# Kernel tuning notes

Measured on AMD Instinct MI355X. Metric: run time of the kernel, lower is better.

Reference implementation:

```python
import jax, jax.numpy as jnp
import numpy as np

N_LAYERS = 3
NUM_USERS = 100000
NUM_ITEMS = 50000
N_NODES = NUM_USERS + NUM_ITEMS
N_EDGES = 6000000
EMB = 64


def setup_inputs() -> dict:
    key = jax.random.key(0)
    k1, k2, k3, k4, k5, k6, k7 = jax.random.split(key, 7)
    user_indices = jax.random.randint(k1, (1024,), 0, NUM_USERS)
    item_indices = jax.random.randint(k2, (1024,), 0, NUM_ITEMS)
    adj_src = jax.random.randint(k3, (N_EDGES,), 0, N_NODES)
    adj_dst = jax.random.randint(k4, (N_EDGES,), 0, N_NODES)
    # normalized adjacency values (stand-in for D^-1/2 A D^-1/2 entries)
    adj_vals = jax.random.uniform(k5, (N_EDGES,), dtype=jnp.float32) * 0.05
    user_emb = jax.random.normal(k6, (NUM_USERS, EMB), dtype=jnp.float32) * 0.1
    item_emb = jax.random.normal(k7, (NUM_ITEMS, EMB), dtype=jnp.float32) * 0.1
    return {
        "user_indices": user_indices,
        "item_indices": item_indices,
        "adj_src": adj_src,
        "adj_dst": adj_dst,
        "adj_vals": adj_vals,
        "user_emb": user_emb,
        "item_emb": item_emb,
    }


def reference(user_indices, item_indices, adj_src, adj_dst, adj_vals, user_emb, item_emb):
    # LightGCN.computer(): all_emb = cat(users, items); repeated SpMM; mean over layers
    all_emb = jnp.concatenate([user_emb, item_emb], axis=0)  # [N, d]
    n = all_emb.shape[0]
    cur = all_emb
    acc = all_emb  # running sum over layer embeddings (fused, avoids stacking)
    for _ in range(N_LAYERS):
        # SpMM in COO form: out[dst] += val * cur[src]
        msgs = adj_vals[:, None] * cur[adj_src]  # [E, d]
        cur = jax.ops.segment_sum(msgs, adj_dst, num_segments=n)
        acc = acc + cur
    light_out = acc / jnp.float32(N_LAYERS + 1)  # mean over (n_layers+1) embeddings
    # forward() returns cat(all_users, all_items) == light_out
    return light_out
```

## Files before the change

### kernel.cpp

```cpp
#include <hip/hip_runtime.h>


#define NUM_USERS 100000
#define NUM_ITEMS 50000
#define N_NODES   150000
#define EMB       64
#define N_EDGES   6000000

#define ROWS_PER_B 256
#define NBUCKETS   586
#define NROWS_PAD  (NBUCKETS * ROWS_PER_B)
#define PART_BLOCKS 512
#define CHUNK ((N_EDGES + PART_BLOCKS - 1) / PART_BLOCKS)
#define CAP_B 10952

constexpr int NODE_F4 = N_NODES * EMB / 4;
constexpr int USER_F4 = NUM_USERS * EMB / 4;

typedef float f4v __attribute__((ext_vector_type(4)));

__device__ __forceinline__ float bf2f(unsigned short u) {
    union { unsigned int i; float f; } x; x.i = ((unsigned int)u) << 16; return x.f;
}
__device__ __forceinline__ unsigned short f2bf(float f) {
    union { float f; unsigned int i; } x; x.f = f;
    unsigned int b = x.i;
    return (unsigned short)((b + 0x7FFFu + ((b >> 16) & 1u)) >> 16);
}


__global__ void k_ginit(int* __restrict__ gcur) {
    int i = blockIdx.x * blockDim.x + threadIdx.x;
    if (i < NBUCKETS) gcur[i] = i * CAP_B;
}

__global__ __launch_bounds__(256) void k_part(const int* __restrict__ src,
                                              const int* __restrict__ dst,
                                              const float* __restrict__ val,
                                              int* __restrict__ gcur,
                                              int2* __restrict__ pairs) {
    __shared__ int cnt[NBUCKETS];
    __shared__ int base[NBUCKETS];
    int t = threadIdx.x;
    for (int i = t; i < NBUCKETS; i += 256) cnt[i] = 0;
    __syncthreads();
    int e0 = blockIdx.x * CHUNK;
    int e1 = min(e0 + CHUNK, N_EDGES);
    {
        int e = e0 + t;
        for (; e + 7 * 256 < e1; e += 8 * 256) {
            int b_[8];
#pragma unroll
            for (int j = 0; j < 8; ++j)
                b_[j] = __builtin_nontemporal_load(dst + e + j * 256) >> 8;
#pragma unroll
            for (int j = 0; j < 8; ++j) atomicAdd(&cnt[b_[j]], 1);
        }
        for (; e < e1; e += 256)
            atomicAdd(&cnt[__builtin_nontemporal_load(dst + e) >> 8], 1);
    }
    __syncthreads();
    for (int i = t; i < NBUCKETS; i += 256) {
        int c = cnt[i];
        base[i] = c ? atomicAdd(&gcur[i], c) : 0;
        cnt[i] = 0;
    }
    __syncthreads();
    {
        int e = e0 + t;
        for (; e + 7 * 256 < e1; e += 8 * 256) {
            int d_[8], s_[8];
            float v_[8];
#pragma unroll
            for (int j = 0; j < 8; ++j)
                d_[j] = __builtin_nontemporal_load(dst + e + j * 256);
#pragma unroll
            for (int j = 0; j < 8; ++j)
                s_[j] = __builtin_nontemporal_load(src + e + j * 256);
#pragma unroll
            for (int j = 0; j < 8; ++j)
                v_[j] = __builtin_nontemporal_load(val + e + j * 256);
#pragma unroll
            for (int j = 0; j < 8; ++j) {
                int b_ = d_[j] >> 8;
                int o = atomicAdd(&cnt[b_], 1);
                pairs[base[b_] + o] = make_int2(s_[j] | ((d_[j] & 255) << 18),
                                                __float_as_int(v_[j]));
            }
        }
        for (; e < e1; e += 256) {
            int d0 = __builtin_nontemporal_load(dst + e);
            int s0 = __builtin_nontemporal_load(src + e);
            float v0 = __builtin_nontemporal_load(val + e);
            int b_ = d0 >> 8;
            int o0 = atomicAdd(&cnt[b_], 1);
            pairs[base[b_] + o0] = make_int2(s0 | ((d0 & 255) << 18),
                                             __float_as_int(v0));
        }
    }
}

__global__ void k_fill(const int* __restrict__ gcur, int* __restrict__ boff) {
    __shared__ int s[1024];
    int t = threadIdx.x;
    int x = (t < NBUCKETS) ? (gcur[t] - t * CAP_B) : 0;
    s[t] = x;
    __syncthreads();
    for (int off = 1; off < 1024; off <<= 1) {
        int v = (t >= off) ? s[t - off] : 0;
        __syncthreads();
        s[t] += v;
        __syncthreads();
    }
    if (t < NBUCKETS) boff[t] = s[t] - x;
    if (t == 0) boff[NBUCKETS] = N_EDGES;
}

__global__ __launch_bounds__(1024) void k_sortA(const int* __restrict__ gcur,
                                                const int* __restrict__ boff,
                                                const int2* __restrict__ pairs1,
                                                int2* __restrict__ pairs2,
                                                int* __restrict__ row_ptr) {
    __shared__ int cnt[ROWS_PER_B];
    __shared__ int s[ROWS_PER_B];
    int b = blockIdx.x;
    int t = threadIdx.x;
    if (t < ROWS_PER_B) cnt[t] = 0;
    __syncthreads();
    int beg = b * CAP_B;
    int end = gcur[b];
    {
        int e = beg + t;
        for (; e + 7 * 1024 < end; e += 8 * 1024) {
            int r_[8];
#pragma unroll
            for (int j = 0; j < 8; ++j)
                r_[j] = ((unsigned)pairs1[e + j * 1024].x) >> 18;
#pragma unroll
            for (int j = 0; j < 8; ++j) atomicAdd(&cnt[r_[j]], 1);
        }
        for (; e < end; e += 1024)
            atomicAdd(&cnt[((unsigned)pairs1[e].x) >> 18], 1);
    }
    __syncthreads();
    int x = (t < ROWS_PER_B) ? cnt[t] : 0;
    if (t < ROWS_PER_B) s[t] = x;
    __syncthreads();
    for (int off = 1; off < ROWS_PER_B; off <<= 1) {
        int v = (t >= off && t < ROWS_PER_B) ? s[t - off] : 0;
        __syncthreads();
        if (t < ROWS_PER_B) s[t] += v;
        __syncthreads();
    }
    if (t < ROWS_PER_B) {
        int ex = boff[b] + s[t] - x;
        row_ptr[b * ROWS_PER_B + t] = ex;
        cnt[t] = ex;
    }
    if (b == NBUCKETS - 1 && t == 0) row_ptr[NROWS_PAD] = N_EDGES;
    __syncthreads();
    const long* p1l = (const long*)pairs1;
    {
        int e = beg + t;
        for (; e + 7 * 1024 < end; e += 8 * 1024) {
            long q[8];
#pragma unroll
            for (int j = 0; j < 8; ++j)
                q[j] = __builtin_nontemporal_load(p1l + e + j * 1024);
#pragma unroll
            for (int j = 0; j < 8; ++j) {
                int x0 = (int)q[j], y0 = (int)(q[j] >> 32);
                int pos = atomicAdd(&cnt[((unsigned)x0) >> 18], 1);
                pairs2[pos] = make_int2(x0 & 0x3FFFF, y0);
            }
        }
        for (; e < end; e += 1024) {
            long q0 = __builtin_nontemporal_load(p1l + e);
            int x0 = (int)q0, y0 = (int)(q0 >> 32);
            int pos = atomicAdd(&cnt[((unsigned)x0) >> 18], 1);
            pairs2[pos] = make_int2(x0 & 0x3FFFF, y0);
        }
    }
}


__global__ void k_zero(int* __restrict__ p, int n) {
    int i = blockIdx.x * blockDim.x + threadIdx.x;
    if (i < n) p[i] = 0;
}

__global__ __launch_bounds__(256) void k_bhist(const int* __restrict__ dst,
                                               int* __restrict__ gcnt,
                                               int* __restrict__ cnt_pb) {
    __shared__ int cnt[NBUCKETS];
    int t = threadIdx.x;
    for (int i = t; i < NBUCKETS; i += 256) cnt[i] = 0;
    __syncthreads();
    int e0 = blockIdx.x * CHUNK;
    int e1 = min(e0 + CHUNK, N_EDGES);
    int e = e0 + t;
    for (; e + 7 * 256 < e1; e += 8 * 256) {
        int b_[8];
#pragma unroll
        for (int j = 0; j < 8; ++j)
            b_[j] = __builtin_nontemporal_load(dst + e + j * 256) >> 8;
#pragma unroll
        for (int j = 0; j < 8; ++j) atomicAdd(&cnt[b_[j]], 1);
    }
    for (; e < e1; e += 256)
        atomicAdd(&cnt[__builtin_nontemporal_load(dst + e) >> 8], 1);
    __syncthreads();
    for (int i = t; i < NBUCKETS; i += 256) {
        int c = cnt[i];
        cnt_pb[blockIdx.x * NBUCKETS + i] = c;
        if (c) atomicAdd(&gcnt[i], c);
    }
}

__global__ void k_bscan(const int* __restrict__ gcnt, int* __restrict__ boff) {
    __shared__ int s[1024];
    int t = threadIdx.x;
    int x = (t < NBUCKETS) ? gcnt[t] : 0;
    s[t] = x;
    __syncthreads();
    for (int off = 1; off < 1024; off <<= 1) {
        int v = (t >= off) ? s[t - off] : 0;
        __syncthreads();
        s[t] += v;
        __syncthreads();
    }
    if (t < NBUCKETS) boff[t] = s[t] - x;
    if (t == 0) boff[NBUCKETS] = N_EDGES;
}

__global__ __launch_bounds__(512) void k_pscan(const int* __restrict__ boff,
                                               int* __restrict__ cnt_pb) {
    __shared__ int s[PART_BLOCKS];
    int k = blockIdx.x;
    int t = threadIdx.x;
    int x = cnt_pb[t * NBUCKETS + k];
    s[t] = x;
    __syncthreads();
    for (int off = 1; off < PART_BLOCKS; off <<= 1) {
        int v = (t >= off) ? s[t - off] : 0;
        __syncthreads();
        s[t] += v;
        __syncthreads();
    }
    cnt_pb[t * NBUCKETS + k] = boff[k] + s[t] - x;
}

__global__ __launch_bounds__(256) void k_part2(const int* __restrict__ src,
                                               const int* __restrict__ dst,
                                               const float* __restrict__ val,
                                               const int* __restrict__ cnt_pb,
                                               int2* __restrict__ pairs) {
    __shared__ int cnt[NBUCKETS];
    __shared__ int base[NBUCKETS];
    int t = threadIdx.x;
    for (int i = t; i < NBUCKETS; i += 256) {
        base[i] = cnt_pb[blockIdx.x * NBUCKETS + i];
        cnt[i] = 0;
    }
    __syncthreads();
    int e0 = blockIdx.x * CHUNK;
    int e1 = min(e0 + CHUNK, N_EDGES);
    int e = e0 + t;
    for (; e + 7 * 256 < e1; e += 8 * 256) {
        int d_[8], s_[8];
        float v_[8];
#pragma unroll
        for (int j = 0; j < 8; ++j)
            d_[j] = __builtin_nontemporal_load(dst + e + j * 256);
#pragma unroll
        for (int j = 0; j < 8; ++j)
            s_[j] = __builtin_nontemporal_load(src + e + j * 256);
#pragma unroll
        for (int j = 0; j < 8; ++j)
            v_[j] = __builtin_nontemporal_load(val + e + j * 256);
#pragma unroll
        for (int j = 0; j < 8; ++j) {
            int b_ = d_[j] >> 8;
            int o = atomicAdd(&cnt[b_], 1);
            pairs[base[b_] + o] = make_int2(s_[j] | ((d_[j] & 255) << 18),
                                            __float_as_int(v_[j]));
        }
    }
    for (; e < e1; e += 256) {
        int d0 = __builtin_nontemporal_load(dst + e);
        int s0 = __builtin_nontemporal_load(src + e);
        float v0 = __builtin_nontemporal_load(val + e);
        int b_ = d0 >> 8;
        int o0 = atomicAdd(&cnt[b_], 1);
        pairs[base[b_] + o0] = make_int2(s0 | ((d0 & 255) << 18),
                                         __float_as_int(v0));
    }
}

__global__ __launch_bounds__(512) void k_sort(const int* __restrict__ boff,
                                              const int2* __restrict__ pairs1,
                                              int2* __restrict__ pairs2,
                                              int* __restrict__ row_ptr) {
    __shared__ int cnt[ROWS_PER_B];
    __shared__ int s[ROWS_PER_B];
    int b = blockIdx.x;
    int t = threadIdx.x;
    if (t < ROWS_PER_B) cnt[t] = 0;
    __syncthreads();
    int beg = boff[b], end = boff[b + 1];
    {
        int e = beg + t;
        for (; e + 7 * 512 < end; e += 8 * 512) {
            int r_[8];
#pragma unroll
            for (int j = 0; j < 8; ++j)
                r_[j] = ((unsigned)pairs1[e + j * 512].x) >> 18;
#pragma unroll
            for (int j = 0; j < 8; ++j) atomicAdd(&cnt[r_[j]], 1);
        }
        for (; e < end; e += 512)
            atomicAdd(&cnt[((unsigned)pairs1[e].x) >> 18], 1);
    }
    __syncthreads();
    int x = (t < ROWS_PER_B) ? cnt[t] : 0;
    if (t < ROWS_PER_B) s[t] = x;
    __syncthreads();
    for (int off = 1; off < ROWS_PER_B; off <<= 1) {
        int v = (t >= off && t < ROWS_PER_B) ? s[t - off] : 0;
        __syncthreads();
        if (t < ROWS_PER_B) s[t] += v;
        __syncthreads();
    }
    if (t < ROWS_PER_B) {
        int ex = beg + s[t] - x;
        row_ptr[b * ROWS_PER_B + t] = ex;
        cnt[t] = ex;
    }
    if (b == NBUCKETS - 1 && t == 0) row_ptr[NROWS_PAD] = N_EDGES;
    __syncthreads();
    const long* p1l = (const long*)pairs1;
    {
        int e = beg + t;
        for (; e + 7 * 512 < end; e += 8 * 512) {
            long q[8];
#pragma unroll
            for (int j = 0; j < 8; ++j)
                q[j] = __builtin_nontemporal_load(p1l + e + j * 512);
#pragma unroll
            for (int j = 0; j < 8; ++j) {
                int x0 = (int)q[j], y0 = (int)(q[j] >> 32);
                int pos = atomicAdd(&cnt[((unsigned)x0) >> 18], 1);
                pairs2[pos] = make_int2(x0 & 0x3FFFF, y0);
            }
        }
        for (; e < end; e += 512) {
            long q0 = __builtin_nontemporal_load(p1l + e);
            int x0 = (int)q0, y0 = (int)(q0 >> 32);
            int pos = atomicAdd(&cnt[((unsigned)x0) >> 18], 1);
            pairs2[pos] = make_int2(x0 & 0x3FFFF, y0);
        }
    }
}


__global__ void k_init(const f4v* __restrict__ ue, const f4v* __restrict__ ie,
                       ushort4* __restrict__ e0b, f4v* __restrict__ acc) {
    int i = blockIdx.x * blockDim.x + threadIdx.x;
    if (i >= NODE_F4) return;
    f4v v = (i < USER_F4) ? __builtin_nontemporal_load(ue + i)
                          : __builtin_nontemporal_load(ie + i - USER_F4);
    __builtin_nontemporal_store(v, acc + i);
    e0b[i] = make_ushort4(f2bf(v.x), f2bf(v.y), f2bf(v.z), f2bf(v.w));
}

__global__ __launch_bounds__(256) void k_spmm(const int* __restrict__ row_ptr,
                                              const long* __restrict__ pairs,
                                              const ushort4* __restrict__ cur,
                                              ushort4* __restrict__ nxt) {
    int tid = blockIdx.x * blockDim.x + threadIdx.x;
    int row = tid >> 4;
    if (row >= N_NODES) return;
    int c = tid & 15;
    int beg = row_ptr[row];
    int end = row_ptr[row + 1];
    float4 r = make_float4(0.f, 0.f, 0.f, 0.f);
    int k = beg;
    for (; k + 7 < end; k += 8) {
        long p[8];
        ushort4 g[8];
#pragma unroll
        for (int j = 0; j < 8; ++j) p[j] = pairs[k + j];
#pragma unroll
        for (int j = 0; j < 8; ++j) g[j] = cur[(long)(int)(p[j] & 0x3FFFF) * 16 + c];
#pragma unroll
        for (int j = 0; j < 8; ++j) {
            float v = __int_as_float((int)(p[j] >> 32));
            r.x += v * bf2f(g[j].x);
            r.y += v * bf2f(g[j].y);
            r.z += v * bf2f(g[j].z);
            r.w += v * bf2f(g[j].w);
        }
    }
    for (; k < end; ++k) {
        long p0 = pairs[k];
        ushort4 g0 = cur[(long)(int)(p0 & 0x3FFFF) * 16 + c];
        float v0 = __int_as_float((int)(p0 >> 32));
        r.x += v0 * bf2f(g0.x);
        r.y += v0 * bf2f(g0.y);
        r.z += v0 * bf2f(g0.z);
        r.w += v0 * bf2f(g0.w);
    }
    nxt[(long)row * 16 + c] = make_ushort4(f2bf(r.x), f2bf(r.y), f2bf(r.z), f2bf(r.w));
}

__global__ __launch_bounds__(256) void k_spmm_fin(const int* __restrict__ row_ptr,
                                                  const long* __restrict__ pairs,
                                                  const ushort4* __restrict__ cur,
                                                  const ushort4* __restrict__ e1b,
                                                  float4* __restrict__ acc) {
    int tid = blockIdx.x * blockDim.x + threadIdx.x;
    int row = tid >> 4;
    if (row >= N_NODES) return;
    int c = tid & 15;
    int beg = row_ptr[row];
    int end = row_ptr[row + 1];
    float4 r = make_float4(0.f, 0.f, 0.f, 0.f);
    int k = beg;
    for (; k + 7 < end; k += 8) {
        long p[8];
        ushort4 g[8];
#pragma unroll
        for (int j = 0; j < 8; ++j) p[j] = pairs[k + j];
#pragma unroll
        for (int j = 0; j < 8; ++j) g[j] = cur[(long)(int)(p[j] & 0x3FFFF) * 16 + c];
#pragma unroll
        for (int j = 0; j < 8; ++j) {
            float v = __int_as_float((int)(p[j] >> 32));
            r.x += v * bf2f(g[j].x);
            r.y += v * bf2f(g[j].y);
            r.z += v * bf2f(g[j].z);
            r.w += v * bf2f(g[j].w);
        }
    }
    for (; k < end; ++k) {
        long p0 = pairs[k];
        ushort4 g0 = cur[(long)(int)(p0 & 0x3FFFF) * 16 + c];
        float v0 = __int_as_float((int)(p0 >> 32));
        r.x += v0 * bf2f(g0.x);
        r.y += v0 * bf2f(g0.y);
        r.z += v0 * bf2f(g0.z);
        r.w += v0 * bf2f(g0.w);
    }
    long o = (long)row * 16 + c;
    ushort4 e1 = e1b[o];
    ushort4 e2 = cur[o];
    float4 a = acc[o];
    a.x = (a.x + bf2f(e1.x) + bf2f(e2.x) + r.x) * 0.25f;
    a.y = (a.y + bf2f(e1.y) + bf2f(e2.y) + r.y) * 0.25f;
    a.z = (a.z + bf2f(e1.z) + bf2f(e2.z) + r.z) * 0.25f;
    a.w = (a.w + bf2f(e1.w) + bf2f(e2.w) + r.w) * 0.25f;
    acc[o] = a;
}


__global__ void lgcn_init(const float4* __restrict__ user_emb,
                          const float4* __restrict__ item_emb,
                          float4* __restrict__ cur, float4* __restrict__ nxt,
                          float4* __restrict__ acc) {
    int i = blockIdx.x * blockDim.x + threadIdx.x;
    if (i >= NODE_F4) return;
    float4 v = (i < USER_F4) ? user_emb[i] : item_emb[i - USER_F4];
    cur[i] = v; acc[i] = v; nxt[i] = make_float4(0.f, 0.f, 0.f, 0.f);
}

__global__ void lgcn_scatter(const int* __restrict__ src, const int* __restrict__ dst,
                             const float* __restrict__ val,
                             const float4* __restrict__ cur, float* __restrict__ nxt) {
    int tid = blockIdx.x * blockDim.x + threadIdx.x;
    int e = tid >> 4;
    if (e >= N_EDGES) return;
    int c = tid & 15;
    int s = src[e]; int d = dst[e]; float v = val[e];
    float4 m = cur[(long)s * 16 + c];
    float* p = nxt + (long)d * 64 + c * 4;
    unsafeAtomicAdd(p + 0, v * m.x);
    unsafeAtomicAdd(p + 1, v * m.y);
    unsafeAtomicAdd(p + 2, v * m.z);
    unsafeAtomicAdd(p + 3, v * m.w);
}

__global__ void lgcn_add_zero(float4* __restrict__ acc, const float4* __restrict__ nxt,
                              float4* __restrict__ other) {
    int i = blockIdx.x * blockDim.x + threadIdx.x;
    if (i >= NODE_F4) return;
    float4 a = acc[i]; float4 n = nxt[i];
    a.x += n.x; a.y += n.y; a.z += n.z; a.w += n.w;
    acc[i] = a;
    other[i] = make_float4(0.f, 0.f, 0.f, 0.f);
}

__global__ void lgcn_final(float4* __restrict__ acc, const float4* __restrict__ nxt) {
    int i = blockIdx.x * blockDim.x + threadIdx.x;
    if (i >= NODE_F4) return;
    float4 a = acc[i]; float4 n = nxt[i];
    a.x = (a.x + n.x) * 0.25f; a.y = (a.y + n.y) * 0.25f;
    a.z = (a.z + n.z) * 0.25f; a.w = (a.w + n.w) * 0.25f;
    acc[i] = a;
}


extern "C" void kernel_launch(void* const* d_in, const int* in_sizes, int n_in,
                              void* d_out, int out_size, void* d_ws, size_t ws_size,
                              hipStream_t stream) {
    const int*    adj_src  = (const int*)d_in[2];
    const int*    adj_dst  = (const int*)d_in[3];
    const float*  adj_vals = (const float*)d_in[4];
    float* acc = (float*)d_out;

    const int BLK = 256;
    const int grid_node  = (NODE_F4 + BLK - 1) / BLK;
    const int grid_row16 = (N_NODES * 16 + BLK - 1) / BLK;

    const size_t SZ_PAIRS = (size_t)N_EDGES * 8;
    const size_t SZ_P1PAD = (size_t)NBUCKETS * CAP_B * 8;
    const size_t SZ_BF    = (size_t)N_NODES * EMB * 2;
    const size_t SZ_RP    = 600320;
    const size_t SZ_B     = 4096;
    const size_t NEEDED1  = SZ_PAIRS + SZ_P1PAD + SZ_BF + SZ_RP + 2 * SZ_B;
    const size_t NEEDED2  = 2 * SZ_PAIRS + SZ_BF + SZ_RP + 3 * SZ_B;

    if (ws_size >= NEEDED1) {
        char* w = (char*)d_ws;
        int2*    pairs2 = (int2*)(w);
        int2*    pairs1 = (int2*)(w + SZ_PAIRS);
        ushort4* e0b    = (ushort4*)(w + SZ_PAIRS);
        ushort4* e1b    = (ushort4*)(w + SZ_PAIRS + SZ_BF);
        ushort4* e2b    = (ushort4*)(w + SZ_PAIRS + SZ_P1PAD);
        int*  row_ptr= (int*)(w + SZ_PAIRS + SZ_P1PAD + SZ_BF);
        int*  gcur   = (int*)(w + SZ_PAIRS + SZ_P1PAD + SZ_BF + SZ_RP);
        int*  boff   = (int*)(w + SZ_PAIRS + SZ_P1PAD + SZ_BF + SZ_RP + SZ_B);

        k_ginit<<<(NBUCKETS + BLK - 1) / BLK, BLK, 0, stream>>>(gcur);
        k_part<<<PART_BLOCKS, BLK, 0, stream>>>(adj_src, adj_dst, adj_vals,
                                                gcur, pairs1);
        k_fill<<<1, 1024, 0, stream>>>(gcur, boff);
        k_sortA<<<NBUCKETS, 1024, 0, stream>>>(gcur, boff, pairs1, pairs2, row_ptr);

        k_init<<<grid_node, BLK, 0, stream>>>((const f4v*)d_in[5], (const f4v*)d_in[6],
                                              e0b, (f4v*)acc);
        k_spmm<<<grid_row16, BLK, 0, stream>>>(row_ptr, (const long*)pairs2, e0b, e1b);
        k_spmm<<<grid_row16, BLK, 0, stream>>>(row_ptr, (const long*)pairs2, e1b, e2b);
        k_spmm_fin<<<grid_row16, BLK, 0, stream>>>(row_ptr, (const long*)pairs2, e2b,
                                                   e1b, (float4*)acc);
    } else if (ws_size >= NEEDED2) {
        char* w = (char*)d_ws;
        int2*    pairs2 = (int2*)(w);
        int*     cnt_pb = (int*)(w);
        int2*    pairs1 = (int2*)(w + SZ_PAIRS);
        ushort4* e0b    = (ushort4*)(w + SZ_PAIRS);
        ushort4* e1b    = (ushort4*)(w + SZ_PAIRS + SZ_BF);
        ushort4* e2b    = (ushort4*)(w + 2 * SZ_PAIRS);
        int*  row_ptr= (int*)(w + 2 * SZ_PAIRS + SZ_BF);
        int*  gcnt   = (int*)(w + 2 * SZ_PAIRS + SZ_BF + SZ_RP);
        int*  boff   = (int*)(w + 2 * SZ_PAIRS + SZ_BF + SZ_RP + SZ_B);

        k_zero<<<(NBUCKETS + BLK - 1) / BLK, BLK, 0, stream>>>(gcnt, NBUCKETS);
        k_bhist<<<PART_BLOCKS, BLK, 0, stream>>>(adj_dst, gcnt, cnt_pb);
        k_bscan<<<1, 1024, 0, stream>>>(gcnt, boff);
        k_pscan<<<NBUCKETS, PART_BLOCKS, 0, stream>>>(boff, cnt_pb);
        k_part2<<<PART_BLOCKS, BLK, 0, stream>>>(adj_src, adj_dst, adj_vals,
                                                 cnt_pb, pairs1);
        k_sort<<<NBUCKETS, 512, 0, stream>>>(boff, pairs1, pairs2, row_ptr);

        k_init<<<grid_node, BLK, 0, stream>>>((const f4v*)d_in[5], (const f4v*)d_in[6],
                                              e0b, (f4v*)acc);
        k_spmm<<<grid_row16, BLK, 0, stream>>>(row_ptr, (const long*)pairs2, e0b, e1b);
        k_spmm<<<grid_row16, BLK, 0, stream>>>(row_ptr, (const long*)pairs2, e1b, e2b);
        k_spmm_fin<<<grid_row16, BLK, 0, stream>>>(row_ptr, (const long*)pairs2, e2b,
                                                   e1b, (float4*)acc);
    } else {
        const float4* user_emb = (const float4*)d_in[5];
        const float4* item_emb = (const float4*)d_in[6];
        float* ws0 = (float*)d_ws;
        float* ws1 = ws0 + (size_t)N_NODES * EMB;
        lgcn_init<<<grid_node, BLK, 0, stream>>>(user_emb, item_emb,
                                                 (float4*)ws0, (float4*)ws1, (float4*)acc);
        lgcn_scatter<<<(N_EDGES*16+BLK-1)/BLK, BLK, 0, stream>>>(adj_src, adj_dst, adj_vals,
                                                    (const float4*)ws0, ws1);
        lgcn_add_zero<<<grid_node, BLK, 0, stream>>>((float4*)acc, (const float4*)ws1, (float4*)ws0);
        lgcn_scatter<<<(N_EDGES*16+BLK-1)/BLK, BLK, 0, stream>>>(adj_src, adj_dst, adj_vals,
                                                    (const float4*)ws1, ws0);
        lgcn_add_zero<<<grid_node, BLK, 0, stream>>>((float4*)acc, (const float4*)ws0, (float4*)ws1);
        lgcn_scatter<<<(N_EDGES*16+BLK-1)/BLK, BLK, 0, stream>>>(adj_src, adj_dst, adj_vals,
                                                    (const float4*)ws0, ws1);
        lgcn_final<<<grid_node, BLK, 0, stream>>>((float4*)acc, (const float4*)ws1);
    }
}
```

Measured before the change: 607.3 us.

## Sort rows by degree within each bucket to balance SpMM wavefront work

The bucket sort kernel now counting-sorts the 256 rows of each bucket by descending degree, with real rows placed before padding rows. It lays out the CSR segments in that sorted order and stores each row's original index in the top 8 bits of row_ptr. The SpMM kernels mask off the offset, recover the original row and write their output there. The aim is for the four 16-lane row groups in a wavefront to have similar edge counts, so fewer lanes sit idle waiting on the longest row. The cost is extra scans and syncs in the sort kernel, plus non-sequential output writes within each bucket.

```diff
diff --git a/kernel.cpp b/kernel.cpp
--- a/kernel.cpp
+++ b/kernel.cpp
@@ -13,6 +13,7 @@
 #define PART_BLOCKS 512
 #define CHUNK ((N_EDGES + PART_BLOCKS - 1) / PART_BLOCKS)
 #define CAP_B 10952
+#define RPMASK 0xFFFFFF
 
 constexpr int NODE_F4 = N_NODES * EMB / 4;
 constexpr int USER_F4 = NUM_USERS * EMB / 4;
@@ -123,6 +124,11 @@
                                                 int* __restrict__ row_ptr) {
     __shared__ int cnt[ROWS_PER_B];
     __shared__ int s[ROWS_PER_B];
+    __shared__ int deg[ROWS_PER_B];
+    __shared__ int sperm[ROWS_PER_B];
+    __shared__ int spos[ROWS_PER_B];
+    __shared__ int dcur[ROWS_PER_B];
+    __shared__ int start[ROWS_PER_B];
     int b = blockIdx.x;
     int t = threadIdx.x;
     if (t < ROWS_PER_B) cnt[t] = 0;
@@ -143,8 +149,19 @@
             atomicAdd(&cnt[((unsigned)pairs1[e].x) >> 18], 1);
     }
     __syncthreads();
-    int x = (t < ROWS_PER_B) ? cnt[t] : 0;
-    if (t < ROWS_PER_B) s[t] = x;
+    int ik = 0;
+    if (t < ROWS_PER_B) {
+        deg[t] = cnt[t];
+        dcur[t] = 0;
+    }
+    __syncthreads();
+    if (t < ROWS_PER_B) {
+        int isreal = (b * ROWS_PER_B + t) < N_NODES;
+        ik = 255 - ((min(deg[t], 127) << 1) | isreal);
+        atomicAdd(&dcur[ik], 1);
+    }
+    __syncthreads();
+    if (t < ROWS_PER_B) s[t] = dcur[t];
     __syncthreads();
     for (int off = 1; off < ROWS_PER_B; off <<= 1) {
         int v = (t >= off && t < ROWS_PER_B) ? s[t - off] : 0;
@@ -152,12 +169,30 @@
         if (t < ROWS_PER_B) s[t] += v;
         __syncthreads();
     }
+    if (t < ROWS_PER_B) dcur[t] = s[t] - dcur[t];
+    __syncthreads();
     if (t < ROWS_PER_B) {
-        int ex = boff[b] + s[t] - x;
-        row_ptr[b * ROWS_PER_B + t] = ex;
-        cnt[t] = ex;
+        int p = atomicAdd(&dcur[ik], 1);
+        sperm[p] = t;
+        spos[t] = p;
+    }
+    __syncthreads();
+    if (t < ROWS_PER_B) s[t] = deg[sperm[t]];
+    __syncthreads();
+    for (int off = 1; off < ROWS_PER_B; off <<= 1) {
+        int v = (t >= off && t < ROWS_PER_B) ? s[t - off] : 0;
+        __syncthreads();
+        if (t < ROWS_PER_B) s[t] += v;
+        __syncthreads();
+    }
+    if (t < ROWS_PER_B) {
+        int st = boff[b] + s[t] - deg[sperm[t]];
+        start[t] = st;
+        row_ptr[b * ROWS_PER_B + t] = st | (sperm[t] << 24);
     }
     if (b == NBUCKETS - 1 && t == 0) row_ptr[NROWS_PAD] = N_EDGES;
+    __syncthreads();
+    if (t < ROWS_PER_B) cnt[t] = start[spos[t]];
     __syncthreads();
     const long* p1l = (const long*)pairs1;
     {
@@ -333,7 +368,7 @@
     }
     if (t < ROWS_PER_B) {
         int ex = beg + s[t] - x;
-        row_ptr[b * ROWS_PER_B + t] = ex;
+        row_ptr[b * ROWS_PER_B + t] = ex | (t << 24);
         cnt[t] = ex;
     }
     if (b == NBUCKETS - 1 && t == 0) row_ptr[NROWS_PAD] = N_EDGES;
@@ -381,8 +416,11 @@
     int row = tid >> 4;
     if (row >= N_NODES) return;
     int c = tid & 15;
-    int beg = row_ptr[row];
-    int end = row_ptr[row + 1];
+    unsigned rp0 = ((const unsigned*)row_ptr)[row];
+    unsigned rp1 = ((const unsigned*)row_ptr)[row + 1];
+    int beg = (int)(rp0 & RPMASK);
+    int end = (int)(rp1 & RPMASK);
+    int orow = (row & ~(ROWS_PER_B - 1)) | (int)(rp0 >> 24);
     float4 r = make_float4(0.f, 0.f, 0.f, 0.f);
     int k = beg;
     for (; k + 7 < end; k += 8) {
@@ -410,7 +448,7 @@
         r.z += v0 * bf2f(g0.z);
         r.w += v0 * bf2f(g0.w);
     }
-    nxt[(long)row * 16 + c] = make_ushort4(f2bf(r.x), f2bf(r.y), f2bf(r.z), f2bf(r.w));
+    nxt[(long)orow * 16 + c] = make_ushort4(f2bf(r.x), f2bf(r.y), f2bf(r.z), f2bf(r.w));
 }
 
 __global__ __launch_bounds__(256) void k_spmm_fin(const int* __restrict__ row_ptr,
@@ -422,8 +460,11 @@
     int row = tid >> 4;
     if (row >= N_NODES) return;
     int c = tid & 15;
-    int beg = row_ptr[row];
-    int end = row_ptr[row + 1];
+    unsigned rp0 = ((const unsigned*)row_ptr)[row];
+    unsigned rp1 = ((const unsigned*)row_ptr)[row + 1];
+    int beg = (int)(rp0 & RPMASK);
+    int end = (int)(rp1 & RPMASK);
+    int orow = (row & ~(ROWS_PER_B - 1)) | (int)(rp0 >> 24);
     float4 r = make_float4(0.f, 0.f, 0.f, 0.f);
     int k = beg;
     for (; k + 7 < end; k += 8) {
@@ -451,7 +492,7 @@
         r.z += v0 * bf2f(g0.z);
         r.w += v0 * bf2f(g0.w);
     }
-    long o = (long)row * 16 + c;
+    long o = (long)orow * 16 + c;
     ushort4 e1 = e1b[o];
     ushort4 e2 = cur[o];
     float4 a = acc[o];
```

Result: slower. 649.6 us (+7.0%).
